# Performance work log

Hardware: AMD Instinct MI355X
Metric: run time of the kernel (lower is better)

Reference implementation:

```python
import jax, jax.numpy as jnp
import numpy as np
import math
from jax import lax

DIM = 128
D_STATE = 16
D_CONV = 4
EXPAND = 2
NSLICES = 16
D_INNER = EXPAND * DIM          # 256
DT_RANK = math.ceil(DIM / 16)   # 8
B_, H_, W_ = 4, 64, 64
L = H_ * W_                     # 4096


def silu(x):
    return x * jax.nn.sigmoid(x)


def causal_conv1d(x, w, b):
    # x: (b, d, l), w: (d, k) depthwise, b: (d,)  -- causal, output length l
    l = x.shape[-1]
    xp = jnp.pad(x, ((0, 0), (0, 0), (D_CONV - 1, 0)))
    y = sum(w[None, :, k, None] * xp[:, :, k:k + l] for k in range(D_CONV))
    return y + b[None, :, None]


def selective_scan(u, delta, A, B, C):
    # u, delta: (b, d, l); A: (d, n); B, C: (b, n, l)
    bsz, d, l = u.shape
    n = A.shape[1]
    u_t = u.transpose(2, 0, 1)      # (l, b, d)
    d_t = delta.transpose(2, 0, 1)  # (l, b, d)
    B_t = B.transpose(2, 0, 1)      # (l, b, n)
    C_t = C.transpose(2, 0, 1)      # (l, b, n)

    def step(h, inp):
        u_, de_, b_, c_ = inp
        dA = jnp.exp(de_[..., None] * A)                    # (b, d, n)
        h = h * dA + (de_ * u_)[..., None] * b_[:, None, :]  # (b, d, n)
        y = jnp.einsum('bdn,bn->bd', h, c_)
        return h, y

    h0 = jnp.zeros((bsz, d, n), u.dtype)
    _, ys = lax.scan(step, h0, (u_t, d_t, B_t, C_t))
    return ys.transpose(1, 2, 0)  # (b, d, l)


def mamba_dir(xz, conv_w, conv_b, x_proj_w, dt_w, dt_b, A_log, Dp):
    # one directional Mamba branch (conv + S6 scan + silu(z) gating), returns (b, d_inner, l)
    x, z = jnp.split(xz, 2, axis=1)
    x = silu(causal_conv1d(x, conv_w, conv_b))
    x_dbl = jnp.einsum('rd,bdl->brl', x_proj_w, x)          # (b, dt_rank+2n, l)
    dt_raw = x_dbl[:, :DT_RANK]
    Bm = x_dbl[:, DT_RANK:DT_RANK + D_STATE]
    Cm = x_dbl[:, DT_RANK + D_STATE:]
    delta = jax.nn.softplus(jnp.einsum('dr,brl->bdl', dt_w, dt_raw) + dt_b[None, :, None])
    A = -jnp.exp(A_log)
    y = selective_scan(x, delta, A, Bm, Cm)
    y = y + Dp[None, :, None] * x
    return y * silu(z)


def setup_inputs() -> dict:
    key = jax.random.key(0)
    ks = iter(jax.random.split(key, 40))

    def rn(shape, scale=0.02):
        return jax.random.normal(next(ks), shape, dtype=jnp.float32) * scale

    inp = {"x_in": jax.random.normal(next(ks), (B_, H_, W_, DIM), dtype=jnp.float32)}
    inp["in_proj_w"] = rn((2 * D_INNER, DIM))
    for suf in ["", "_b", "_s"]:
        inp["conv_w" + suf] = rn((D_INNER, D_CONV), 0.1)
        inp["conv_b" + suf] = rn((D_INNER,), 0.1)
        inp["x_proj_w" + suf] = rn((DT_RANK + 2 * D_STATE, D_INNER))
        inp["dt_proj_w" + suf] = rn((D_INNER, DT_RANK), 0.1)
        inp["dt_proj_b" + suf] = rn((D_INNER,), 0.1)
        inp["A_log" + suf] = jnp.log(jnp.tile(jnp.arange(1, D_STATE + 1, dtype=jnp.float32), (D_INNER, 1)))
        inp["D" + suf] = jnp.ones((D_INNER,), jnp.float32)
    inp["out_proj_w"] = rn((DIM, D_INNER))
    return inp


def reference(x_in, in_proj_w, conv_w, conv_b, x_proj_w, dt_proj_w, dt_proj_b, A_log, D,
              conv_w_b, conv_b_b, x_proj_w_b, dt_proj_w_b, dt_proj_b_b, A_log_b, D_b,
              conv_w_s, conv_b_s, x_proj_w_s, dt_proj_w_s, dt_proj_b_s, A_log_s, D_s,
              out_proj_w):
    b, h, w, c = x_in.shape
    l = h * w
    x = x_in.reshape(b, l, c)
    xz = jnp.einsum('pd,bld->bpl', in_proj_w, x)  # (b, 2*d_inner, l)

    # forward scan
    y_f = mamba_dir(xz, conv_w, conv_b, x_proj_w, dt_proj_w, dt_proj_b, A_log, D)
    # backward scan (flip along length)
    y_b = jnp.flip(mamba_dir(jnp.flip(xz, -1), conv_w_b, conv_b_b, x_proj_w_b,
                             dt_proj_w_b, dt_proj_b_b, A_log_b, D_b), -1)
    # interleaved-slice scan: chunk length into NSLICES pieces, stack, flatten
    m = l // NSLICES
    xz_s = xz.reshape(b, 2 * D_INNER, NSLICES, m).swapaxes(-1, -2).reshape(b, 2 * D_INNER, l)
    y_s = mamba_dir(xz_s, conv_w_s, conv_b_s, x_proj_w_s, dt_proj_w_s, dt_proj_b_s, A_log_s, D_s)
    y_s = y_s.reshape(b, D_INNER, m, NSLICES).swapaxes(-1, -2).reshape(b, D_INNER, l)

    y = y_f + y_b + y_s
    out = jnp.einsum('od,bdl->blo', out_proj_w, y)
    return out.reshape(b, h, w, c)
```

## Files before the change

### kernel.cpp

```cpp
#include <hip/hip_runtime.h>
#include <math.h>

#define LSEQ 4096

#define XZ_OFF   0ULL
#define XZ_SZ    (4ULL * 4096 * 512)
#define U_OFF    (XZ_OFF + XZ_SZ)
#define DIR_SZ   (4ULL * 256 * 4096)
#define DELTA_OFF (U_OFF + 3ULL * DIR_SZ)
#define BC_OFF   (DELTA_OFF + 3ULL * DIR_SZ)
#define BC_SZ    (4ULL * 4096 * 32)
#define WTIN_OFF DELTA_OFF
#define WTOUT_OFF U_OFF

typedef float v2f __attribute__((ext_vector_type(2)));
typedef float v4f __attribute__((ext_vector_type(4)));

__device__ __forceinline__ float sigmoidf_(float x) { return 1.0f / (1.0f + __expf(-x)); }
__device__ __forceinline__ float siluf_(float x)    { return x * sigmoidf_(x); }

__device__ __forceinline__ float fast_exp2_asm(float x) {
    float r;
    asm volatile("v_exp_f32 %0, %1\n\ts_nop 0" : "=v"(r) : "v"(x));
    return r;
}
#if defined(__has_builtin)
#if __has_builtin(__builtin_amdgcn_exp2f)
#define EXP2(x) __builtin_amdgcn_exp2f(x)
#else
#define EXP2(x) fast_exp2_asm(x)
#endif
#else
#define EXP2(x) fast_exp2_asm(x)
#endif

__device__ __forceinline__ float softplus_fast(float x) {
    float t = EXP2(1.44269504f * x);
    float r = 0.69314718f * __log2f(1.0f + t);
    return (x > 20.0f) ? x : r;
}

__device__ __forceinline__ int perm_idx(int dir, int j) {
    if (dir == 0) return j;
    if (dir == 1) return 4095 - j;
    return ((j & 15) << 8) | (j >> 4);
}

#define DPP_MOV(x, ctrl) __int_as_float(__builtin_amdgcn_update_dpp(0, __float_as_int(x), (ctrl), 0xF, 0xF, true))

__global__ __launch_bounds__(256) void transpose_in_kernel(const float* __restrict__ w,
                                                           float* __restrict__ wT) {
    int idx = blockIdx.x * 256 + threadIdx.x;
    int p = idx >> 7, c = idx & 127;
    wT[(size_t)c * 512 + p] = w[(size_t)p * 128 + c];
}

__global__ __launch_bounds__(256) void inproj_kernel(const float* __restrict__ x,
                              const float* __restrict__ wT,
                              float* __restrict__ xz) {
    const int b = blockIdx.y;
    const int l0 = blockIdx.x * 16;
    __shared__ float xs[128 * 20];
    for (int idx = threadIdx.x; idx < 16 * 128; idx += 256) {
        int li = idx >> 7, c = idx & 127;
        xs[c * 20 + li] = x[((size_t)(b * 4096 + l0 + li)) * 128 + c];
    }
    __syncthreads();
    const int p0 = (threadIdx.x & 127) * 4;
    const int g8 = (threadIdx.x >> 7) * 8;
    float acc[4][8];
    #pragma unroll
    for (int j = 0; j < 4; ++j)
        #pragma unroll
        for (int k = 0; k < 8; ++k) acc[j][k] = 0.0f;
    for (int c = 0; c < 128; ++c) {
        float4 wv = *(const float4*)(wT + (size_t)c * 512 + p0);
        const float* xp = xs + c * 20 + g8;
        float4 x0 = *(const float4*)(xp);
        float4 x1 = *(const float4*)(xp + 4);
        float xv[8] = {x0.x, x0.y, x0.z, x0.w, x1.x, x1.y, x1.z, x1.w};
        float wj[4] = {wv.x, wv.y, wv.z, wv.w};
        #pragma unroll
        for (int j = 0; j < 4; ++j)
            #pragma unroll
            for (int k = 0; k < 8; ++k) acc[j][k] += wj[j] * xv[k];
    }
    #pragma unroll
    for (int k = 0; k < 8; ++k) {
        float4 s; s.x = acc[0][k]; s.y = acc[1][k]; s.z = acc[2][k]; s.w = acc[3][k];
        *(float4*)(xz + ((size_t)(b * 4096 + l0 + g8 + k)) * 512 + p0) = s;
    }
}

__global__ __launch_bounds__(256) void front_kernel(float* __restrict__ ws,
        const float* __restrict__ xw0, const float* __restrict__ xw1, const float* __restrict__ xw2,
        const float* __restrict__ dw0, const float* __restrict__ dw1, const float* __restrict__ dw2,
        const float* __restrict__ db0, const float* __restrict__ db1, const float* __restrict__ db2,
        const float* __restrict__ cw0, const float* __restrict__ cb0,
        const float* __restrict__ cw1, const float* __restrict__ cb1,
        const float* __restrict__ cw2, const float* __restrict__ cb2) {
    const int l0 = blockIdx.x * 32, b = blockIdx.y, dir = blockIdx.z;
    const float* xw = (dir == 0) ? xw0 : (dir == 1) ? xw1 : xw2;
    const float* dw = (dir == 0) ? dw0 : (dir == 1) ? dw1 : dw2;
    const float* db = (dir == 0) ? db0 : (dir == 1) ? db1 : db2;
    const float* cw = (dir == 0) ? cw0 : (dir == 1) ? cw1 : cw2;
    const float* cb = (dir == 0) ? cb0 : (dir == 1) ? cb1 : cb2;
    const float* xzb = ws + XZ_OFF + (size_t)b * 4096 * 512;
    float* ub      = ws + U_OFF + (size_t)dir * DIR_SZ + (size_t)b * 256 * 4096;
    float* deltab  = ws + DELTA_OFF + (size_t)dir * DIR_SZ + (size_t)b * 256 * 4096;
    float* Bf      = ws + BC_OFF + (size_t)dir * BC_SZ;
    float* Cf      = Bf + BC_SZ / 2;

    __shared__ float xt[35 * 260];
    __shared__ float xd[40 * 33];
    __shared__ float xws[40 * 68];
    float* ut = xt;

    for (int idx = threadIdx.x; idx < 35 * 64; idx += 256) {
        int k = idx >> 6, dq = idx & 63;
        int j = l0 - 3 + k;
        float4 v = {0.f, 0.f, 0.f, 0.f};
        if (j >= 0) {
            int row = (dir == 0) ? j : (dir == 1) ? (4095 - j) : (((j & 15) << 8) | (j >> 4));
            v = *(const float4*)(xzb + (size_t)row * 512 + dq * 4);
        }
        *(float4*)(xt + k * 260 + dq * 4) = v;
    }
    __syncthreads();

    const int d = threadIdx.x;
    const float w0 = cw[d * 4 + 0], w1 = cw[d * 4 + 1], w2 = cw[d * 4 + 2], w3 = cw[d * 4 + 3];
    const float bb = cb[d];
    float win[35];
    #pragma unroll
    for (int k = 0; k < 35; ++k) win[k] = xt[k * 260 + d];
    float r[32];
    #pragma unroll
    for (int li = 0; li < 32; ++li)
        r[li] = siluf_(bb + w0 * win[li] + w1 * win[li + 1] + w2 * win[li + 2] + w3 * win[li + 3]);
    {
        float* urow = ub + (size_t)d * 4096 + l0;
        #pragma unroll
        for (int q = 0; q < 8; ++q) {
            float4 v; v.x = r[q*4]; v.y = r[q*4+1]; v.z = r[q*4+2]; v.w = r[q*4+3];
            *(float4*)(urow + q * 4) = v;
        }
    }
    __syncthreads();

    #pragma unroll
    for (int li = 0; li < 32; ++li)
        ut[li * 264 + 4 * (((d >> 2) ^ (li & 7))) + (d & 3)] = r[li];

    {
        const int rg = threadIdx.x >> 5;
        const int li = threadIdx.x & 31;
        float acc[5];
        #pragma unroll
        for (int j = 0; j < 5; ++j) acc[j] = 0.0f;
        const float* up = ut + li * 264;
        const int sw = (li & 7);
        for (int ct = 0; ct < 4; ++ct) {
            __syncthreads();
            for (int idx = threadIdx.x; idx < 40 * 16; idx += 256) {
                int rr = idx >> 4, q = (idx & 15) * 4;
                *(float4*)(xws + rr * 68 + q) = *(const float4*)(xw + (size_t)rr * 256 + ct * 64 + q);
            }
            __syncthreads();
            #pragma unroll 4
            for (int c4t = 0; c4t < 16; ++c4t) {
                const int cc = 4 * (c4t ^ sw);
                float4 uv = *(const float4*)(up + ct * 64 + cc);
                #pragma unroll
                for (int j = 0; j < 5; ++j) {
                    float4 wv = *(const float4*)(xws + (rg * 5 + j) * 68 + cc);
                    acc[j] += wv.x * uv.x + wv.y * uv.y + wv.z * uv.z + wv.w * uv.w;
                }
            }
        }
        #pragma unroll
        for (int j = 0; j < 5; ++j) xd[(rg * 5 + j) * 33 + li] = acc[j];
    }
    __syncthreads();

    {
        const int wv = threadIdx.x >> 6;
        const int lane = threadIdx.x & 63;
        const int n = lane >> 2, lq = lane & 3;
        #pragma unroll
        for (int j = 0; j < 2; ++j) {
            int l4 = (l0 >> 2) + j * 4 + wv;
            int li = (j * 4 + wv) * 4 + lq;
            size_t base = (((size_t)b * 1024 + l4) * 16 + n) * 4 + lq;
            Bf[base] = xd[(8 + n) * 33 + li];
            Cf[base] = xd[(24 + n) * 33 + li];
        }
    }
    {
        const int li = threadIdx.x & 31;
        float xr8[8];
        #pragma unroll
        for (int rr = 0; rr < 8; ++rr) xr8[rr] = xd[rr * 33 + li];
        #pragma unroll
        for (int k = 0; k < 32; ++k) {
            int dd = ((threadIdx.x + k * 256) >> 5);
            float4 wa = *(const float4*)(dw + dd * 8);
            float4 wb = *(const float4*)(dw + dd * 8 + 4);
            float acc = db[dd]
                + wa.x * xr8[0] + wa.y * xr8[1] + wa.z * xr8[2] + wa.w * xr8[3]
                + wb.x * xr8[4] + wb.y * xr8[5] + wb.z * xr8[6] + wb.w * xr8[7];
            deltab[(size_t)dd * 4096 + l0 + li] = softplus_fast(acc);
        }
    }
}

__global__ __launch_bounds__(512, 8) void scan_kernel(float* __restrict__ ws,
                            const float* __restrict__ Al0, const float* __restrict__ Dp0,
                            const float* __restrict__ Al1, const float* __restrict__ Dp1,
                            const float* __restrict__ Al2, const float* __restrict__ Dp2) {
    const int d = blockIdx.x, b = blockIdx.y, dir = blockIdx.z;
    const float* Al = (dir == 0) ? Al0 : (dir == 1) ? Al1 : Al2;
    const float* Dp = (dir == 0) ? Dp0 : (dir == 1) ? Dp1 : Dp2;
    const int c = threadIdx.x >> 4;
    const int n = threadIdx.x & 15;
    const int nl = n & 7;
    const float Ane = -1.44269504f * __expf(Al[d * 16 + n]);
    const v2f AneD = {Ane, Ane};
    const float Dd = Dp[d];
    const float* urow = ws + U_OFF + (size_t)dir * DIR_SZ + ((size_t)(b * 256 + d)) * 4096;
    float* drow = ws + DELTA_OFF + (size_t)dir * DIR_SZ + ((size_t)(b * 256 + d)) * 4096;

    __shared__ float sdu[32 * 260];
    __shared__ float ps[1024];
    float* Psh = ps;
    float* Ssh = ps + 512;

    {
        const float4* d4 = (const float4*)drow;
        const float4* u4 = (const float4*)urow;
        for (int i = threadIdx.x; i < 1024; i += 512) {
            float4 dv = d4[i], uv = u4[i];
            int l = i * 4;
            float* p = sdu + (l >> 7) * 260 + (l & 127) * 2;
            *(float4*)(p) = dv; *(float4*)(p + 4) = uv;
        }
    }
    __syncthreads();

    const v4f* Bq = (const v4f*)(ws + BC_OFF + (size_t)dir * BC_SZ)
                       + ((size_t)b * 1024 + c * 32) * 16 + n;
    const v4f* Cq = (const v4f*)(ws + BC_OFF + (size_t)dir * BC_SZ + BC_SZ / 2)
                       + ((size_t)b * 1024 + c * 32) * 16 + n;
    const v4f* sp = (const v4f*)(sdu + c * 260);

    float S = 0.0f;
    v2f ds2 = {0.0f, 0.0f};
    #pragma unroll 8
    for (int k4 = 0; k4 < 32; ++k4) {
        v4f dq = sp[k4 * 2], uq = sp[k4 * 2 + 1];
        v4f Bv = Bq[(size_t)k4 * 16];
        v2f du0 = dq.xy * uq.xy;
        v2f du1 = dq.zw * uq.zw;
        v2f t0 = AneD * dq.xy;
        v2f t1 = AneD * dq.zw;
        v2f p0 = du0 * Bv.xy;
        v2f p1 = du1 * Bv.zw;
        ds2 += dq.xy + dq.zw;
        S = __builtin_fmaf(S, EXP2(t0.x), p0.x);
        S = __builtin_fmaf(S, EXP2(t0.y), p0.y);
        S = __builtin_fmaf(S, EXP2(t1.x), p1.x);
        S = __builtin_fmaf(S, EXP2(t1.y), p1.y);
    }
    Ssh[c * 16 + n] = S;
    Psh[c * 16 + n] = EXP2(Ane * (ds2.x + ds2.y));
    __syncthreads();
    float h = 0.0f;
    #pragma unroll 2
    for (int k = 0; k < c; ++k) h = __builtin_fmaf(h, Psh[k * 16 + n], Ssh[k * 16 + n]);

    #define SCAN_STEP(t, ee, pp, Cn) { \
        h = __builtin_fmaf(h, (ee), (pp)); \
        float yp = h * (Cn); \
        yp += DPP_MOV(yp, 0xB1); \
        yp += DPP_MOV(yp, 0x4E); \
        yp += DPP_MOV(yp, 0x124); \
        yp += DPP_MOV(yp, 0x128); \
        if (nl == (t)) ysel = yp; }

    for (int g = 0; g < 16; ++g) {
        const int j0 = g * 8 + nl;
        float uo = sdu[c * 260 + ((j0 >> 2) << 3) + 4 + (j0 & 3)];
        v4f d0 = sp[g * 4 + 0], u0 = sp[g * 4 + 1];
        v4f d1 = sp[g * 4 + 2], u1 = sp[g * 4 + 3];
        v4f Bv0 = Bq[(size_t)(g * 2) * 16], Bv1 = Bq[(size_t)(g * 2 + 1) * 16];
        v4f Cv0 = Cq[(size_t)(g * 2) * 16], Cv1 = Cq[(size_t)(g * 2 + 1) * 16];
        v2f t0 = AneD * d0.xy, t1 = AneD * d0.zw;
        v2f t2 = AneD * d1.xy, t3 = AneD * d1.zw;
        v2f q0 = d0.xy * u0.xy, q1 = d0.zw * u0.zw;
        v2f q2 = d1.xy * u1.xy, q3 = d1.zw * u1.zw;
        v2f p0 = q0 * Bv0.xy, p1 = q1 * Bv0.zw;
        v2f p2 = q2 * Bv1.xy, p3 = q3 * Bv1.zw;
        float e0 = EXP2(t0.x), e1 = EXP2(t0.y);
        float e2 = EXP2(t1.x), e3 = EXP2(t1.y);
        float e4 = EXP2(t2.x), e5 = EXP2(t2.y);
        float e6 = EXP2(t3.x), e7 = EXP2(t3.y);
        float ysel = 0.0f;
        SCAN_STEP(0, e0, p0.x, Cv0.x)
        SCAN_STEP(1, e1, p0.y, Cv0.y)
        SCAN_STEP(2, e2, p1.x, Cv0.z)
        SCAN_STEP(3, e3, p1.y, Cv0.w)
        SCAN_STEP(4, e4, p2.x, Cv1.x)
        SCAN_STEP(5, e5, p2.y, Cv1.y)
        SCAN_STEP(6, e6, p3.x, Cv1.z)
        SCAN_STEP(7, e7, p3.y, Cv1.w)
        if (n < 8) drow[perm_idx(dir, c * 128 + j0)] = ysel + Dd * uo;
    }
    #undef SCAN_STEP
}

__global__ __launch_bounds__(256) void transpose_w_kernel(const float* __restrict__ ow,
                                                          float* __restrict__ wT) {
    int idx = blockIdx.x * 256 + threadIdx.x;
    int o = idx >> 8, d = idx & 255;
    wT[(size_t)d * 128 + o] = ow[(size_t)o * 256 + d];
}

__global__ __launch_bounds__(256) void epilogue_kernel(const float* __restrict__ ws,
                                const float* __restrict__ wT,
                                float* __restrict__ out) {
    const int l0 = blockIdx.x * 16, b = blockIdx.y;
    __shared__ float yt[256 * 20];
    __shared__ float wts[64 * 128];
    const float* yf = ws + DELTA_OFF;
    const float* yb = ws + DELTA_OFF + DIR_SZ;
    const float* ysd = ws + DELTA_OFF + 2 * DIR_SZ;
    const float* xzb = ws + XZ_OFF + (size_t)b * 4096 * 512;

    for (int idx = threadIdx.x; idx < 256 * 4; idx += 256) {
        int d = idx >> 2, q = (idx & 3) * 4;
        size_t ro = ((size_t)(b * 256 + d)) * 4096 + l0 + q;
        float4 vf = *(const float4*)(yf + ro);
        float4 vb = *(const float4*)(yb + ro);
        float4 vs = *(const float4*)(ysd + ro);
        float4 s; s.x = vf.x + vb.x + vs.x; s.y = vf.y + vb.y + vs.y;
        s.z = vf.z + vb.z + vs.z; s.w = vf.w + vb.w + vs.w;
        *(float4*)(yt + d * 20 + q) = s;
    }
    __syncthreads();
    {
        const int d = threadIdx.x;
        #pragma unroll 4
        for (int li = 0; li < 16; ++li) {
            float z = xzb[(size_t)(l0 + li) * 512 + 256 + d];
            yt[d * 20 + li] *= siluf_(z);
        }
    }

    const int o0 = (threadIdx.x & 31) * 4;
    const int lp = (threadIdx.x >> 5) * 2;
    float a0[4], a1[4];
    #pragma unroll
    for (int j = 0; j < 4; ++j) { a0[j] = 0.0f; a1[j] = 0.0f; }
    for (int dt = 0; dt < 4; ++dt) {
        __syncthreads();
        for (int idx = threadIdx.x; idx < 64 * 32; idx += 256) {
            int dd = idx >> 5, q = (idx & 31) * 4;
            *(float4*)(wts + dd * 128 + q) = *(const float4*)(wT + (size_t)(dt * 64 + dd) * 128 + q);
        }
        __syncthreads();
        #pragma unroll 4
        for (int dl = 0; dl < 64; ++dl) {
            float4 w = *(const float4*)(wts + dl * 128 + o0);
            float2 y = *(const float2*)(yt + (dt * 64 + dl) * 20 + lp);
            a0[0] += w.x * y.x; a0[1] += w.y * y.x; a0[2] += w.z * y.x; a0[3] += w.w * y.x;
            a1[0] += w.x * y.y; a1[1] += w.y * y.y; a1[2] += w.z * y.y; a1[3] += w.w * y.y;
        }
    }
    float4 s0; s0.x = a0[0]; s0.y = a0[1]; s0.z = a0[2]; s0.w = a0[3];
    float4 s1; s1.x = a1[0]; s1.y = a1[1]; s1.z = a1[2]; s1.w = a1[3];
    *(float4*)(out + ((size_t)(b * 4096 + l0 + lp)) * 128 + o0) = s0;
    *(float4*)(out + ((size_t)(b * 4096 + l0 + lp + 1)) * 128 + o0) = s1;
}

extern "C" void kernel_launch(void* const* d_in, const int* in_sizes, int n_in,
                              void* d_out, int out_size, void* d_ws, size_t ws_size,
                              hipStream_t stream) {
    const float* x_in = (const float*)d_in[0];
    const float* ipw  = (const float*)d_in[1];
    const float* cw[3]  = {(const float*)d_in[2],  (const float*)d_in[9],  (const float*)d_in[16]};
    const float* cb[3]  = {(const float*)d_in[3],  (const float*)d_in[10], (const float*)d_in[17]};
    const float* xpw[3] = {(const float*)d_in[4],  (const float*)d_in[11], (const float*)d_in[18]};
    const float* dtw[3] = {(const float*)d_in[5],  (const float*)d_in[12], (const float*)d_in[19]};
    const float* dtb[3] = {(const float*)d_in[6],  (const float*)d_in[13], (const float*)d_in[20]};
    const float* alog[3]= {(const float*)d_in[7],  (const float*)d_in[14], (const float*)d_in[21]};
    const float* dp[3]  = {(const float*)d_in[8],  (const float*)d_in[15], (const float*)d_in[22]};
    const float* ow   = (const float*)d_in[23];
    float* ws  = (float*)d_ws;
    float* out = (float*)d_out;

    transpose_in_kernel<<<dim3(256), 256, 0, stream>>>(ipw, ws + WTIN_OFF);
    inproj_kernel<<<dim3(256, 4), 256, 0, stream>>>(x_in, ws + WTIN_OFF, ws);
    front_kernel<<<dim3(128, 4, 3), 256, 0, stream>>>(ws,
        xpw[0], xpw[1], xpw[2], dtw[0], dtw[1], dtw[2], dtb[0], dtb[1], dtb[2],
        cw[0], cb[0], cw[1], cb[1], cw[2], cb[2]);
    scan_kernel<<<dim3(256, 4, 3), 512, 0, stream>>>(ws,
        alog[0], dp[0], alog[1], dp[1], alog[2], dp[2]);
    transpose_w_kernel<<<dim3(128), 256, 0, stream>>>(ow, ws + WTOUT_OFF);
    epilogue_kernel<<<dim3(256, 4), 256, 0, stream>>>(ws, ws + WTOUT_OFF, out);
}
```

Measured before the change: 361.0 us.

## Process two channels per scan block and restructure the DPP reduction tree

The scan kernel now handles two inner channels per 1024-thread block, with each 16-lane group owning one (channel, chunk) pair and separate shared buffers per channel. The per-step cross-lane reduction of h*C is replaced by a transposed reduction tree: all eight steps are computed first, then partial sums are combined with selects between DPP stages, which cuts the number of DPP ops per group of eight steps and takes them off the serial h-recurrence. The aim is to lower reduction instruction count and latency in the inner loop. The larger blocks double the shared memory per block and the launch-bound change may alter register allocation and occupancy.

```diff
diff --git a/kernel.cpp b/kernel.cpp
--- a/kernel.cpp
+++ b/kernel.cpp
@@ -214,36 +214,36 @@
     }
 }
 
-__global__ __launch_bounds__(512, 8) void scan_kernel(float* __restrict__ ws,
+__global__ __launch_bounds__(1024, 8) void scan_kernel(float* __restrict__ ws,
                             const float* __restrict__ Al0, const float* __restrict__ Dp0,
                             const float* __restrict__ Al1, const float* __restrict__ Dp1,
                             const float* __restrict__ Al2, const float* __restrict__ Dp2) {
-    const int d = blockIdx.x, b = blockIdx.y, dir = blockIdx.z;
+    const int d0 = blockIdx.x * 2, b = blockIdx.y, dir = blockIdx.z;
     const float* Al = (dir == 0) ? Al0 : (dir == 1) ? Al1 : Al2;
     const float* Dp = (dir == 0) ? Dp0 : (dir == 1) ? Dp1 : Dp2;
-    const int c = threadIdx.x >> 4;
-    const int n = threadIdx.x & 15;
+    const int n  = threadIdx.x & 15;
+    const int d2 = (threadIdx.x >> 4) & 1;
+    const int c  = threadIdx.x >> 5;
     const int nl = n & 7;
+    const int d = d0 + d2;
     const float Ane = -1.44269504f * __expf(Al[d * 16 + n]);
     const v2f AneD = {Ane, Ane};
     const float Dd = Dp[d];
-    const float* urow = ws + U_OFF + (size_t)dir * DIR_SZ + ((size_t)(b * 256 + d)) * 4096;
-    float* drow = ws + DELTA_OFF + (size_t)dir * DIR_SZ + ((size_t)(b * 256 + d)) * 4096;
-
-    __shared__ float sdu[32 * 260];
-    __shared__ float ps[1024];
-    float* Psh = ps;
-    float* Ssh = ps + 512;
-
-    {
-        const float4* d4 = (const float4*)drow;
-        const float4* u4 = (const float4*)urow;
-        for (int i = threadIdx.x; i < 1024; i += 512) {
-            float4 dv = d4[i], uv = u4[i];
-            int l = i * 4;
-            float* p = sdu + (l >> 7) * 260 + (l & 127) * 2;
-            *(float4*)(p) = dv; *(float4*)(p + 4) = uv;
-        }
+    const float* ubase = ws + U_OFF + (size_t)dir * DIR_SZ + ((size_t)(b * 256 + d0)) * 4096;
+    float* dbase = ws + DELTA_OFF + (size_t)dir * DIR_SZ + ((size_t)(b * 256 + d0)) * 4096;
+    const float* urow = ubase + (size_t)d2 * 4096;
+    float* drow = dbase + (size_t)d2 * 4096;
+
+    __shared__ float sdu[2][32 * 260];
+    __shared__ float ps[2][1024];
+
+    for (int i = threadIdx.x; i < 2048; i += 1024) {
+        int dsl = i >> 10, ii = i & 1023;
+        float4 dv = ((const float4*)(dbase + (size_t)dsl * 4096))[ii];
+        float4 uv = ((const float4*)(ubase + (size_t)dsl * 4096))[ii];
+        int l = ii * 4;
+        float* p = sdu[dsl] + (l >> 7) * 260 + (l & 127) * 2;
+        *(float4*)(p) = dv; *(float4*)(p + 4) = uv;
     }
     __syncthreads();
 
@@ -251,7 +251,9 @@
                        + ((size_t)b * 1024 + c * 32) * 16 + n;
     const v4f* Cq = (const v4f*)(ws + BC_OFF + (size_t)dir * BC_SZ + BC_SZ / 2)
                        + ((size_t)b * 1024 + c * 32) * 16 + n;
-    const v4f* sp = (const v4f*)(sdu + c * 260);
+    const v4f* sp = (const v4f*)(sdu[d2] + c * 260);
+    float* Psh = ps[d2];
+    float* Ssh = ps[d2] + 512;
 
     float S = 0.0f;
     v2f ds2 = {0.0f, 0.0f};
@@ -278,44 +280,49 @@
     #pragma unroll 2
     for (int k = 0; k < c; ++k) h = __builtin_fmaf(h, Psh[k * 16 + n], Ssh[k * 16 + n]);
 
-    #define SCAN_STEP(t, ee, pp, Cn) { \
-        h = __builtin_fmaf(h, (ee), (pp)); \
-        float yp = h * (Cn); \
-        yp += DPP_MOV(yp, 0xB1); \
-        yp += DPP_MOV(yp, 0x4E); \
-        yp += DPP_MOV(yp, 0x124); \
-        yp += DPP_MOV(yp, 0x128); \
-        if (nl == (t)) ysel = yp; }
-
     for (int g = 0; g < 16; ++g) {
         const int j0 = g * 8 + nl;
-        float uo = sdu[c * 260 + ((j0 >> 2) << 3) + 4 + (j0 & 3)];
-        v4f d0 = sp[g * 4 + 0], u0 = sp[g * 4 + 1];
-        v4f d1 = sp[g * 4 + 2], u1 = sp[g * 4 + 3];
+        float uo = sdu[d2][c * 260 + ((j0 >> 2) << 3) + 4 + (j0 & 3)];
+        v4f dq0 = sp[g * 4 + 0], uq0 = sp[g * 4 + 1];
+        v4f dq1 = sp[g * 4 + 2], uq1 = sp[g * 4 + 3];
         v4f Bv0 = Bq[(size_t)(g * 2) * 16], Bv1 = Bq[(size_t)(g * 2 + 1) * 16];
         v4f Cv0 = Cq[(size_t)(g * 2) * 16], Cv1 = Cq[(size_t)(g * 2 + 1) * 16];
-        v2f t0 = AneD * d0.xy, t1 = AneD * d0.zw;
-        v2f t2 = AneD * d1.xy, t3 = AneD * d1.zw;
-        v2f q0 = d0.xy * u0.xy, q1 = d0.zw * u0.zw;
-        v2f q2 = d1.xy * u1.xy, q3 = d1.zw * u1.zw;
+        v2f t0 = AneD * dq0.xy, t1 = AneD * dq0.zw;
+        v2f t2 = AneD * dq1.xy, t3 = AneD * dq1.zw;
+        v2f q0 = dq0.xy * uq0.xy, q1 = dq0.zw * uq0.zw;
+        v2f q2 = dq1.xy * uq1.xy, q3 = dq1.zw * uq1.zw;
         v2f p0 = q0 * Bv0.xy, p1 = q1 * Bv0.zw;
         v2f p2 = q2 * Bv1.xy, p3 = q3 * Bv1.zw;
         float e0 = EXP2(t0.x), e1 = EXP2(t0.y);
         float e2 = EXP2(t1.x), e3 = EXP2(t1.y);
         float e4 = EXP2(t2.x), e5 = EXP2(t2.y);
         float e6 = EXP2(t3.x), e7 = EXP2(t3.y);
-        float ysel = 0.0f;
-        SCAN_STEP(0, e0, p0.x, Cv0.x)
-        SCAN_STEP(1, e1, p0.y, Cv0.y)
-        SCAN_STEP(2, e2, p1.x, Cv0.z)
-        SCAN_STEP(3, e3, p1.y, Cv0.w)
-        SCAN_STEP(4, e4, p2.x, Cv1.x)
-        SCAN_STEP(5, e5, p2.y, Cv1.y)
-        SCAN_STEP(6, e6, p3.x, Cv1.z)
-        SCAN_STEP(7, e7, p3.y, Cv1.w)
+        float ya0, ya1, ya2, ya3, ya4, ya5, ya6, ya7;
+        h = __builtin_fmaf(h, e0, p0.x); ya0 = h * Cv0.x;
+        h = __builtin_fmaf(h, e1, p0.y); ya1 = h * Cv0.y;
+        h = __builtin_fmaf(h, e2, p1.x); ya2 = h * Cv0.z;
+        h = __builtin_fmaf(h, e3, p1.y); ya3 = h * Cv0.w;
+        h = __builtin_fmaf(h, e4, p2.x); ya4 = h * Cv1.x;
+        h = __builtin_fmaf(h, e5, p2.y); ya5 = h * Cv1.y;
+        h = __builtin_fmaf(h, e6, p3.x); ya6 = h * Cv1.z;
+        h = __builtin_fmaf(h, e7, p3.y); ya7 = h * Cv1.w;
+        ya0 += DPP_MOV(ya0, 0xB1); ya1 += DPP_MOV(ya1, 0xB1);
+        ya2 += DPP_MOV(ya2, 0xB1); ya3 += DPP_MOV(ya3, 0xB1);
+        ya4 += DPP_MOV(ya4, 0xB1); ya5 += DPP_MOV(ya5, 0xB1);
+        ya6 += DPP_MOV(ya6, 0xB1); ya7 += DPP_MOV(ya7, 0xB1);
+        float z0 = (n & 1) ? ya1 : ya0;
+        float z1 = (n & 1) ? ya3 : ya2;
+        float z2 = (n & 1) ? ya5 : ya4;
+        float z3 = (n & 1) ? ya7 : ya6;
+        z0 += DPP_MOV(z0, 0x4E); z1 += DPP_MOV(z1, 0x4E);
+        z2 += DPP_MOV(z2, 0x4E); z3 += DPP_MOV(z3, 0x4E);
+        float w0 = (n & 2) ? z1 : z0;
+        float w1 = (n & 2) ? z3 : z2;
+        w0 += DPP_MOV(w0, 0x124); w1 += DPP_MOV(w1, 0x124);
+        w0 += DPP_MOV(w0, 0x128); w1 += DPP_MOV(w1, 0x128);
+        float ysel = (n & 4) ? w1 : w0;
         if (n < 8) drow[perm_idx(dir, c * 128 + j0)] = ysel + Dd * uo;
     }
-    #undef SCAN_STEP
 }
 
 __global__ __launch_bounds__(256) void transpose_w_kernel(const float* __restrict__ ow,
@@ -403,7 +410,7 @@
     front_kernel<<<dim3(128, 4, 3), 256, 0, stream>>>(ws,
         xpw[0], xpw[1], xpw[2], dtw[0], dtw[1], dtw[2], dtb[0], dtb[1], dtb[2],
         cw[0], cb[0], cw[1], cb[1], cw[2], cb[2]);
-    scan_kernel<<<dim3(256, 4, 3), 512, 0, stream>>>(ws,
+    scan_kernel<<<dim3(128, 4, 3), 1024, 0, stream>>>(ws,
         alog[0], dp[0], alog[1], dp[1], alog[2], dp[2]);
     transpose_w_kernel<<<dim3(128), 256, 0, stream>>>(ow, ws + WTOUT_OFF);
     epilogue_kernel<<<dim3(256, 4), 256, 0, stream>>>(ws, ws + WTOUT_OFF, out);
```

Result: no change. 363.1 us (+0.6%).
